# Performance work log

Hardware: AMD Instinct MI355X
Metric: run time of the kernel (lower is better)

The kernel has to match this reference:

```python
import jax, jax.numpy as jnp
import numpy as np

DIM = 1024
INNER = int(DIM * 1.5)
EPS = 1e-6


def setup_inputs() -> dict:
    key = jax.random.key(0)
    ks = jax.random.split(key, 8)
    B, L, D = 4, 2048, DIM
    s1 = 1.0 / np.sqrt(D)
    s2 = 1.0 / np.sqrt(INNER)
    return {
        "x": jax.random.normal(ks[0], (B, L, D), jnp.float32),
        "W1": jax.random.normal(ks[1], (D, INNER), jnp.float32) * s1,
        "b1": jnp.zeros((INNER,), jnp.float32),
        "W2": jax.random.normal(ks[2], (INNER, 3 * D), jnp.float32) * s2,
        "b2": jnp.zeros((3 * D,), jnp.float32),
        "Wv": jax.random.normal(ks[3], (D, D), jnp.float32) * (0.5 * s1),
        "bv": jnp.zeros((D,), jnp.float32),
        "mix_weight": jnp.full((D,), 0.5, jnp.float32),
        "norm_weight": jnp.ones((D,), jnp.float32),
    }


def rmsnorm(x, w):
    norm = jnp.sqrt(jnp.mean(x * x, axis=-1, keepdims=True) + EPS)
    return x / norm * w


def reference(x, W1, b1, W2, b2, Wv, bv, mix_weight, norm_weight):
    B, L, D = x.shape
    h = jax.nn.silu(x @ W1 + b1)              # [B,L,inner]
    qkg = h @ W2 + b2                          # [B,L,3D]
    q, k, g = jnp.split(qkg, 3, axis=-1)
    scores = jnp.einsum('bld,bmd->blm', q, k) / jnp.sqrt(jnp.float32(D))
    attn = jax.nn.softmax(scores, axis=-1)
    v = (x @ Wv + bv) * jax.nn.sigmoid(g)      # gated values [B,L,D]
    global_info = jnp.einsum('blm,bmd->bld', attn, v)
    output = mix_weight * global_info + (1.0 - mix_weight) * x
    return rmsnorm(output, norm_weight)
```

## Files before the change

### kernel.cpp

```cpp
#include <hip/hip_runtime.h>
#include <hip/hip_bf16.h>
#include <stdint.h>


typedef __bf16 bf16x8 __attribute__((ext_vector_type(8)));
typedef float f32x4 __attribute__((ext_vector_type(4)));

#define VM4 asm volatile("s_waitcnt vmcnt(4)" ::: "memory")
#define VM2 asm volatile("s_waitcnt vmcnt(2)" ::: "memory")
#define VM0 asm volatile("s_waitcnt vmcnt(0)" ::: "memory")
#define LGKM0 asm volatile("s_waitcnt lgkmcnt(0)" ::: "memory")
#define BAR __builtin_amdgcn_s_barrier()
#define SCB __builtin_amdgcn_sched_barrier(0)

__device__ __forceinline__ unsigned short f2bf(float f) {
    unsigned int u = __float_as_uint(f);
    u += 0x7fffu + ((u >> 16) & 1u);
    return (unsigned short)(u >> 16);
}
__device__ __forceinline__ float bf2f(unsigned short s) {
    return __uint_as_float(((unsigned int)s) << 16);
}
__device__ __forceinline__ void llds16(const void* g, void* l) {
    __builtin_amdgcn_global_load_lds(
        (const __attribute__((address_space(1))) void*)g,
        (__attribute__((address_space(3))) void*)l, 16, 0, 0);
}
__device__ __forceinline__ f32x4 MF(bf16x8 a, bf16x8 b, f32x4 c) {
    return __builtin_amdgcn_mfma_f32_16x16x32_bf16(a, b, c, 0, 0, 0);
}

__global__ __launch_bounds__(256) void cvt_f32_bf16(
    const float* __restrict__ in, unsigned short* __restrict__ out, long long n8) {
    long long i = (long long)blockIdx.x * 256 + threadIdx.x;
    if (i >= n8) return;
    float4 a = ((const float4*)in)[2 * i];
    float4 b = ((const float4*)in)[2 * i + 1];
    ushort4 p0, p1;
    p0.x = f2bf(a.x); p0.y = f2bf(a.y); p0.z = f2bf(a.z); p0.w = f2bf(a.w);
    p1.x = f2bf(b.x); p1.y = f2bf(b.y); p1.z = f2bf(b.z); p1.w = f2bf(b.w);
    ((ushort4*)out)[2 * i] = p0;
    ((ushort4*)out)[2 * i + 1] = p1;
}

__global__ __launch_bounds__(256) void transpose_cvt(
    const float* __restrict__ in, unsigned short* __restrict__ out, int R, int C) {
    __shared__ unsigned short tile[32][33];
    int c0 = blockIdx.x * 32, r0 = blockIdx.y * 32;
    int cc = threadIdx.x & 31, rr = threadIdx.x >> 5;
#pragma unroll
    for (int p = 0; p < 4; ++p) {
        int r = rr + p * 8;
        tile[r][cc] = f2bf(in[(size_t)(r0 + r) * C + c0 + cc]);
    }
    __syncthreads();
#pragma unroll
    for (int p = 0; p < 4; ++p) {
        int c = rr + p * 8;
        out[(size_t)(c0 + c) * R + r0 + cc] = tile[cc][c];
    }
}

template <int EPI>
__global__ __launch_bounds__(512, 1) void gemm5(
    const unsigned short* __restrict__ A, int lda, long long Abs,
    const unsigned short* __restrict__ B, int ldb, long long Bbs,
    int K,
    void* __restrict__ out, int ldo, long long Obs,
    const float* __restrict__ bias,
    const unsigned short* __restrict__ gate, int ldg,
    const float* __restrict__ xres, const float* __restrict__ mix,
    float scale, int gx) {
    __shared__ unsigned short lds[49152];
    const int tid = threadIdx.x, lane = tid & 63, wid = tid >> 6;
    const int wr = wid >> 1, wc = wid & 1;
    const int nwg = gridDim.x;
    const int bswz = ((int)blockIdx.x & 7) * (nwg >> 3) + ((int)blockIdx.x >> 3);
    const int bx = bswz % gx, by = bswz / gx;
    const int bm = by * 256, bn = bx * 128;
    const int z = blockIdx.z;
    A += (long long)z * Abs;
    B += (long long)z * Bbs;
    const int NT = K >> 6;

    const int sswz = ((tid & 7) ^ ((tid >> 3) & 7)) * 8;
    size_t agc[4], bgc[2];
#pragma unroll
    for (int c = 0; c < 4; ++c)
        agc[c] = (size_t)(bm + c * 64 + (tid >> 3)) * lda + sswz;
#pragma unroll
    for (int c = 0; c < 2; ++c)
        bgc[c] = (size_t)(bn + c * 64 + (tid >> 3)) * ldb + sswz;
    const int wl = wid * 512;

    auto stA01 = [&](int t, int buf) {
        const size_t k0 = (size_t)t << 6;
        llds16(A + agc[0] + k0, &lds[buf + wl]);
        llds16(A + agc[1] + k0, &lds[buf + 4096 + wl]);
    };
    auto stA23 = [&](int t, int buf) {
        const size_t k0 = (size_t)t << 6;
        llds16(A + agc[2] + k0, &lds[buf + 8192 + wl]);
        llds16(A + agc[3] + k0, &lds[buf + 12288 + wl]);
    };
    auto stB = [&](int t, int buf) {
        const size_t k0 = (size_t)t << 6;
        llds16(B + bgc[0] + k0, &lds[buf + 16384 + wl]);
        llds16(B + bgc[1] + k0, &lds[buf + 20480 + wl]);
    };

    const int l15 = lane & 15, g4 = lane >> 4, l7 = lane & 7;
    const int x0 = (g4 ^ l7) * 8, x1 = ((4 + g4) ^ l7) * 8;
    const int ab = (wr * 64 + l15) * 64;
    const int bbv = 16384 + (wc * 64 + l15) * 64;
    constexpr int X = 0, Y = 24576;

    f32x4 acc[4][4] = {};

    stB(0, X); stA01(0, X); stA23(0, X); stB(1, Y);
    VM4;
    BAR; SCB;

    int t = 0;
    while (true) {
        const bool last = (t + 2) >= NT;
        bf16x8 bf[4][2], af[2][2];
#pragma unroll
        for (int j = 0; j < 4; ++j) {
            bf[j][0] = *(const bf16x8*)&lds[X + bbv + j * 1024 + x0];
            bf[j][1] = *(const bf16x8*)&lds[X + bbv + j * 1024 + x1];
        }
#pragma unroll
        for (int i = 0; i < 2; ++i) {
            af[i][0] = *(const bf16x8*)&lds[X + ab + i * 1024 + x0];
            af[i][1] = *(const bf16x8*)&lds[X + ab + i * 1024 + x1];
        }
        stA01(t + 1, Y);
        LGKM0; SCB;
        __builtin_amdgcn_s_setprio(1);
#pragma unroll
        for (int s = 0; s < 2; ++s)
#pragma unroll
            for (int i = 0; i < 2; ++i)
#pragma unroll
                for (int j = 0; j < 4; ++j)
                    acc[i][j] = MF(af[i][s], bf[j][s], acc[i][j]);
        __builtin_amdgcn_s_setprio(0);
        VM4;
        BAR; SCB;
#pragma unroll
        for (int i = 0; i < 2; ++i) {
            af[i][0] = *(const bf16x8*)&lds[X + ab + (2 + i) * 1024 + x0];
            af[i][1] = *(const bf16x8*)&lds[X + ab + (2 + i) * 1024 + x1];
        }
        stA23(t + 1, Y);
        if (!last) stB(t + 2, X);
        LGKM0; SCB;
        __builtin_amdgcn_s_setprio(1);
#pragma unroll
        for (int s = 0; s < 2; ++s)
#pragma unroll
            for (int i = 0; i < 2; ++i)
#pragma unroll
                for (int j = 0; j < 4; ++j)
                    acc[2 + i][j] = MF(af[i][s], bf[j][s], acc[2 + i][j]);
        __builtin_amdgcn_s_setprio(0);
        if (last) { VM2; } else { VM4; }
        BAR; SCB;
#pragma unroll
        for (int j = 0; j < 4; ++j) {
            bf[j][0] = *(const bf16x8*)&lds[Y + bbv + j * 1024 + x0];
            bf[j][1] = *(const bf16x8*)&lds[Y + bbv + j * 1024 + x1];
        }
#pragma unroll
        for (int i = 0; i < 2; ++i) {
            af[i][0] = *(const bf16x8*)&lds[Y + ab + i * 1024 + x0];
            af[i][1] = *(const bf16x8*)&lds[Y + ab + i * 1024 + x1];
        }
        if (!last) stA01(t + 2, X);
        LGKM0; SCB;
        __builtin_amdgcn_s_setprio(1);
#pragma unroll
        for (int s = 0; s < 2; ++s)
#pragma unroll
            for (int i = 0; i < 2; ++i)
#pragma unroll
                for (int j = 0; j < 4; ++j)
                    acc[i][j] = MF(af[i][s], bf[j][s], acc[i][j]);
        __builtin_amdgcn_s_setprio(0);
        if (last) { VM0; } else { VM4; }
        BAR; SCB;
#pragma unroll
        for (int i = 0; i < 2; ++i) {
            af[i][0] = *(const bf16x8*)&lds[Y + ab + (2 + i) * 1024 + x0];
            af[i][1] = *(const bf16x8*)&lds[Y + ab + (2 + i) * 1024 + x1];
        }
        if (!last) { stA23(t + 2, X); stB(t + 3, Y); }
        LGKM0; SCB;
        __builtin_amdgcn_s_setprio(1);
#pragma unroll
        for (int s = 0; s < 2; ++s)
#pragma unroll
            for (int i = 0; i < 2; ++i)
#pragma unroll
                for (int j = 0; j < 4; ++j)
                    acc[2 + i][j] = MF(af[i][s], bf[j][s], acc[2 + i][j]);
        __builtin_amdgcn_s_setprio(0);
        if (last) break;
        VM4;
        BAR; SCB;
        t += 2;
    }

    const int row0 = bm + wr * 64, col0 = bn + wc * 64;
#pragma unroll
    for (int i = 0; i < 4; ++i) {
#pragma unroll
        for (int j = 0; j < 4; ++j) {
            const int n = col0 + j * 16 + l15;
            const int mb = row0 + i * 16 + g4 * 4;
            f32x4 v = acc[i][j];
            if constexpr (EPI == 1) {
                float bs = bias[n];
                unsigned short* o = (unsigned short*)out;
#pragma unroll
                for (int q = 0; q < 4; ++q)
                    o[(size_t)(mb + q) * ldo + n] = f2bf(v[q] + bs);
            } else if constexpr (EPI == 2) {
                float bs = bias[n];
                ushort4 pk;
                unsigned short* pku = (unsigned short*)&pk;
#pragma unroll
                for (int q = 0; q < 4; ++q) {
                    int m = mb + q;
                    float g = bf2f(gate[(size_t)m * ldg + n]);
                    pku[q] = f2bf((v[q] + bs) / (1.f + __expf(-g)));
                }
                unsigned short* o = (unsigned short*)out;
                size_t oi = ((size_t)(mb >> 11) * 1024 + n) * 2048 + (mb & 2047);
                *(ushort4*)(o + oi) = pk;
            } else if constexpr (EPI == 3) {
                float* o = (float*)out + (size_t)z * Obs;
#pragma unroll
                for (int q = 0; q < 4; ++q)
                    o[(size_t)(mb + q) * ldo + n] = v[q] * scale;
            } else {
                float* o = (float*)out + (size_t)z * Obs;
                const float* xr = xres + (size_t)z * Obs;
                float mw = mix[n];
#pragma unroll
                for (int q = 0; q < 4; ++q)
                    o[(size_t)(mb + q) * ldo + n] =
                        mw * v[q] + (1.f - mw) * xr[(size_t)(mb + q) * ldo + n];
            }
        }
    }
}

template <int EPI>
__global__ __launch_bounds__(256, 3) void gemmk(
    const unsigned short* __restrict__ A, int lda,
    const unsigned short* __restrict__ B, int ldb,
    int K, void* __restrict__ out, int ldo,
    const float* __restrict__ bias, int gx) {
    __shared__ unsigned short lds[24576];
    const int tid = threadIdx.x, lane = tid & 63, wid = tid >> 6;
    const int nwg = gridDim.x;
    const int bswz = ((int)blockIdx.x & 7) * (nwg >> 3) + ((int)blockIdx.x >> 3);
    const int bx = bswz % gx, by = bswz / gx;
    const int bm = by * 128, bn = bx * 128;
    const int NT = K >> 5;

    const int srow = tid >> 2;
    const int sswz = ((tid & 3) ^ ((tid >> 3) & 3)) * 8;
    size_t ag[2], bg[2];
    ag[0] = (size_t)(bm + srow) * lda + sswz;
    ag[1] = (size_t)(bm + 64 + srow) * lda + sswz;
    bg[0] = (size_t)(bn + srow) * ldb + sswz;
    bg[1] = (size_t)(bn + 64 + srow) * ldb + sswz;
    const int wl = wid * 512;

    auto stage = [&](int t, int bb) {
        const size_t k0 = (size_t)t << 5;
        llds16(A + ag[0] + k0, &lds[bb + wl]);
        llds16(A + ag[1] + k0, &lds[bb + 2048 + wl]);
        llds16(B + bg[0] + k0, &lds[bb + 4096 + wl]);
        llds16(B + bg[1] + k0, &lds[bb + 6144 + wl]);
    };

    const int wr = wid >> 1, wc = wid & 1;
    const int l15 = lane & 15, g4 = lane >> 4;
    const int fswz = (g4 ^ ((l15 >> 1) & 3)) * 8;
    const int aoff = (wr * 64 + l15) * 32 + fswz;
    const int boff = 4096 + (wc * 64 + l15) * 32 + fswz;

    f32x4 acc[4][4] = {};
    stage(0, 0);
    stage(1, 8192);
    VM4; BAR;

    int bb = 0;
    for (int t = 0; t < NT; ++t) {
        const bool st = (t + 2) < NT;
        if (st) {
            const int tgt = (bb >= 8192) ? bb - 8192 : bb + 16384;
            stage(t + 2, tgt);
        }
        SCB;
        bf16x8 af[4], bf[4];
#pragma unroll
        for (int i = 0; i < 4; ++i) {
            af[i] = *(const bf16x8*)&lds[bb + aoff + i * 512];
            bf[i] = *(const bf16x8*)&lds[bb + boff + i * 512];
        }
#pragma unroll
        for (int i = 0; i < 4; ++i)
#pragma unroll
            for (int j = 0; j < 4; ++j)
                acc[i][j] = MF(af[i], bf[j], acc[i][j]);
        LGKM0;
        if (st) { VM4; } else { VM0; }
        BAR;
        bb = (bb == 16384) ? 0 : bb + 8192;
    }

    const int row0 = bm + wr * 64, col0 = bn + wc * 64;
#pragma unroll
    for (int i = 0; i < 4; ++i) {
#pragma unroll
        for (int j = 0; j < 4; ++j) {
            const int n = col0 + j * 16 + l15;
            const int mb = row0 + i * 16 + g4 * 4;
            f32x4 v = acc[i][j];
            float bs = bias[n];
            unsigned short* o = (unsigned short*)out;
#pragma unroll
            for (int q = 0; q < 4; ++q) {
                float val = v[q] + bs;
                if constexpr (EPI == 0) val = val / (1.f + __expf(-val));
                o[(size_t)(mb + q) * ldo + n] = f2bf(val);
            }
        }
    }
}

__global__ __launch_bounds__(256) void softmax_inplace(float* __restrict__ scores) {
    const int L = 2048;
    float* sr = scores + (size_t)blockIdx.x * L;
    const int t = threadIdx.x, lane = t & 63, wid = t >> 6;
    float4 a = ((const float4*)sr)[2 * t];
    float4 b = ((const float4*)sr)[2 * t + 1];
    float vv[8] = {a.x, a.y, a.z, a.w, b.x, b.y, b.z, b.w};
    float mx = vv[0];
#pragma unroll
    for (int i = 1; i < 8; ++i) mx = fmaxf(mx, vv[i]);
#pragma unroll
    for (int off = 32; off; off >>= 1) mx = fmaxf(mx, __shfl_xor(mx, off));
    __shared__ float redm[4], reds[4];
    if (lane == 0) redm[wid] = mx;
    __syncthreads();
    mx = fmaxf(fmaxf(redm[0], redm[1]), fmaxf(redm[2], redm[3]));
    float s = 0.f;
#pragma unroll
    for (int i = 0; i < 8; ++i) {
        vv[i] = __expf(vv[i] - mx);
        s += vv[i];
    }
#pragma unroll
    for (int off = 32; off; off >>= 1) s += __shfl_xor(s, off);
    if (lane == 0) reds[wid] = s;
    __syncthreads();
    s = reds[0] + reds[1] + reds[2] + reds[3];
    float inv = 1.f / s;
    ushort4 p0, p1;
    unsigned short* pp0 = (unsigned short*)&p0;
    unsigned short* pp1 = (unsigned short*)&p1;
#pragma unroll
    for (int i = 0; i < 4; ++i) pp0[i] = f2bf(vv[i] * inv);
#pragma unroll
    for (int i = 0; i < 4; ++i) pp1[i] = f2bf(vv[4 + i] * inv);
    unsigned short* pr = (unsigned short*)sr;
    ((ushort4*)pr)[2 * t] = p0;
    ((ushort4*)pr)[2 * t + 1] = p1;
}

__global__ __launch_bounds__(256) void rmsnorm_inplace(
    float* __restrict__ io, const float* __restrict__ w) {
    const int D = 1024;
    float* r = io + (size_t)blockIdx.x * D;
    const int t = threadIdx.x, lane = t & 63, wid = t >> 6;
    float4 v = ((const float4*)r)[t];
    float ss = v.x * v.x + v.y * v.y + v.z * v.z + v.w * v.w;
#pragma unroll
    for (int off = 32; off; off >>= 1) ss += __shfl_xor(ss, off);
    __shared__ float red[4];
    if (lane == 0) red[wid] = ss;
    __syncthreads();
    ss = red[0] + red[1] + red[2] + red[3];
    float sc = rsqrtf(ss / (float)D + 1e-6f);
    float4 wv = ((const float4*)w)[t];
    v.x *= sc * wv.x; v.y *= sc * wv.y; v.z *= sc * wv.z; v.w *= sc * wv.w;
    ((float4*)r)[t] = v;
}

extern "C" void kernel_launch(void* const* d_in, const int* in_sizes, int n_in,
                              void* d_out, int out_size, void* d_ws, size_t ws_size,
                              hipStream_t stream) {
    const float* x = (const float*)d_in[0];
    const float* W1 = (const float*)d_in[1];
    const float* b1 = (const float*)d_in[2];
    const float* W2 = (const float*)d_in[3];
    const float* b2 = (const float*)d_in[4];
    const float* Wv = (const float*)d_in[5];
    const float* bv = (const float*)d_in[6];
    const float* mixw = (const float*)d_in[7];
    const float* normw = (const float*)d_in[8];
    float* out = (float*)d_out;

    const int L = 2048, D = 1024, INNER = 1536, BN4 = 4;
    const int M = BN4 * L;

    char* w = (char*)d_ws;
    auto carve = [&](size_t bytes) {
        void* p = (void*)w;
        w += (bytes + 255) & ~(size_t)255;
        return p;
    };
    unsigned short* xbf = (unsigned short*)carve((size_t)M * D * 2);
    unsigned short* w1t = (unsigned short*)carve((size_t)INNER * D * 2);
    unsigned short* w2t = (unsigned short*)carve((size_t)3 * D * INNER * 2);
    unsigned short* wvt = (unsigned short*)carve((size_t)D * D * 2);
    unsigned short* h = (unsigned short*)carve((size_t)M * INNER * 2);
    unsigned short* qkg = (unsigned short*)carve((size_t)M * 3 * D * 2);
    unsigned short* vt = (unsigned short*)carve((size_t)BN4 * D * L * 2);
    float* scores = (float*)carve((size_t)BN4 * L * L * 4);

    cvt_f32_bf16<<<(M * D) / 2048, 256, 0, stream>>>(x, xbf, (long long)M * D / 8);
    transpose_cvt<<<dim3(INNER / 32, D / 32), 256, 0, stream>>>(W1, w1t, D, INNER);
    transpose_cvt<<<dim3(3 * D / 32, INNER / 32), 256, 0, stream>>>(W2, w2t, INNER, 3 * D);
    transpose_cvt<<<dim3(D / 32, D / 32), 256, 0, stream>>>(Wv, wvt, D, D);
    gemmk<0><<<dim3(768, 1, 1), 256, 0, stream>>>(xbf, D, w1t, D, D, h, INNER,
                                                  b1, 12);
    gemm5<1><<<dim3(768, 1, 1), 512, 0, stream>>>(
        h, INNER, 0, w2t, INNER, 0, INNER, qkg, 3 * D, 0, b2, nullptr, 0,
        nullptr, nullptr, 1.f, 24);
    gemm5<2><<<dim3(256, 1, 1), 512, 0, stream>>>(
        xbf, D, 0, wvt, D, 0, D, vt, L, 0, bv, qkg + 2 * D, 3 * D, nullptr,
        nullptr, 1.f, 8);
    gemm5<3><<<dim3(128, 1, BN4), 512, 0, stream>>>(
        qkg, 3 * D, (long long)L * 3 * D, qkg + D, 3 * D, (long long)L * 3 * D,
        D, scores, L, (long long)L * L, nullptr, nullptr, 0, nullptr, nullptr,
        0.03125f, 16);
    softmax_inplace<<<BN4 * L, 256, 0, stream>>>(scores);
    gemm5<4><<<dim3(64, 1, BN4), 512, 0, stream>>>(
        (const unsigned short*)scores, 2 * L, (long long)L * 2 * L, vt, L,
        (long long)D * L, L, out, D, (long long)L * D, nullptr, nullptr, 0, x,
        mixw, 1.f, 8);
    rmsnorm_inplace<<<M, 256, 0, stream>>>(out, normw);
}
```

Measured before the change: 291.1 us.

## Fuse softmax into QK and PV GEMM epilogues using Cauchy-Schwarz max bound

Removes the separate softmax kernel and the fp32 score matrix. The QKG GEMM epilogue now accumulates per-row squared norms of q and k with atomics. A small kernel turns these into a per-batch upper bound on the scores (max|q|·max|k|/sqrt(D)). The QK GEMM then writes exp(score - bound) directly as bf16 and atomically accumulates row sums, and the PV GEMM divides by the row sum in its epilogue. This saves a full fp32 write, read and rewrite of the 4x2048x2048 score matrix. The risk is exp underflow when the bound is loose compared with the actual row max, plus atomic contention and the extra zeroing and bounds launches.

```diff
diff --git a/kernel.cpp b/kernel.cpp
--- a/kernel.cpp
+++ b/kernel.cpp
@@ -28,6 +28,11 @@
 }
 __device__ __forceinline__ f32x4 MF(bf16x8 a, bf16x8 b, f32x4 c) {
     return __builtin_amdgcn_mfma_f32_16x16x32_bf16(a, b, c, 0, 0, 0);
+}
+
+__global__ __launch_bounds__(256) void zero_f32(float* __restrict__ p, int n) {
+    int i = blockIdx.x * 256 + threadIdx.x;
+    if (i < n) p[i] = 0.f;
 }
 
 __global__ __launch_bounds__(256) void cvt_f32_bf16(
@@ -61,6 +66,30 @@
     }
 }
 
+__global__ __launch_bounds__(256) void bounds_kernel(
+    const float* __restrict__ nrm, float* __restrict__ bounds) {
+    const int z = blockIdx.x, t = threadIdx.x;
+    float qm = 0.f, km = 0.f;
+    for (int i = t; i < 2048; i += 256) {
+        qm = fmaxf(qm, nrm[z * 2048 + i]);
+        km = fmaxf(km, nrm[8192 + z * 2048 + i]);
+    }
+#pragma unroll
+    for (int off = 32; off; off >>= 1) {
+        qm = fmaxf(qm, __shfl_xor(qm, off));
+        km = fmaxf(km, __shfl_xor(km, off));
+    }
+    __shared__ float rq[4], rk[4];
+    const int lane = t & 63, wid = t >> 6;
+    if (lane == 0) { rq[wid] = qm; rk[wid] = km; }
+    __syncthreads();
+    if (t == 0) {
+        qm = fmaxf(fmaxf(rq[0], rq[1]), fmaxf(rq[2], rq[3]));
+        km = fmaxf(fmaxf(rk[0], rk[1]), fmaxf(rk[2], rk[3]));
+        bounds[z] = sqrtf(qm) * sqrtf(km) * 0.03125f;
+    }
+}
+
 template <int EPI>
 __global__ __launch_bounds__(512, 1) void gemm5(
     const unsigned short* __restrict__ A, int lda, long long Abs,
@@ -70,7 +99,8 @@
     const float* __restrict__ bias,
     const unsigned short* __restrict__ gate, int ldg,
     const float* __restrict__ xres, const float* __restrict__ mix,
-    float scale, int gx) {
+    float scale, int gx,
+    const float* __restrict__ bnd, float* __restrict__ stat) {
     __shared__ unsigned short lds[49152];
     const int tid = threadIdx.x, lane = tid & 63, wid = tid >> 6;
     const int wr = wid >> 1, wc = wid & 1;
@@ -213,45 +243,99 @@
     }
 
     const int row0 = bm + wr * 64, col0 = bn + wc * 64;
-#pragma unroll
-    for (int i = 0; i < 4; ++i) {
-#pragma unroll
-        for (int j = 0; j < 4; ++j) {
-            const int n = col0 + j * 16 + l15;
+    if constexpr (EPI == 1) {
+        unsigned short* o = (unsigned short*)out;
+        const int seg = col0 >> 10;
+#pragma unroll
+        for (int i = 0; i < 4; ++i) {
             const int mb = row0 + i * 16 + g4 * 4;
-            f32x4 v = acc[i][j];
-            if constexpr (EPI == 1) {
-                float bs = bias[n];
-                unsigned short* o = (unsigned short*)out;
-#pragma unroll
-                for (int q = 0; q < 4; ++q)
-                    o[(size_t)(mb + q) * ldo + n] = f2bf(v[q] + bs);
-            } else if constexpr (EPI == 2) {
-                float bs = bias[n];
+            float ssq[4] = {0.f, 0.f, 0.f, 0.f};
+#pragma unroll
+            for (int j = 0; j < 4; ++j) {
+                const int n = col0 + j * 16 + l15;
+                const float bs = bias[n];
+#pragma unroll
+                for (int q = 0; q < 4; ++q) {
+                    float val = acc[i][j][q] + bs;
+                    o[(size_t)(mb + q) * ldo + n] = f2bf(val);
+                    ssq[q] += val * val;
+                }
+            }
+            if (seg < 2) {
+#pragma unroll
+                for (int q = 0; q < 4; ++q) {
+                    float s = ssq[q];
+                    s += __shfl_xor(s, 1); s += __shfl_xor(s, 2);
+                    s += __shfl_xor(s, 4); s += __shfl_xor(s, 8);
+                    if (l15 == 0) atomicAdd(&stat[seg * 8192 + mb + q], s);
+                }
+            }
+        }
+    } else if constexpr (EPI == 2) {
+        unsigned short* o = (unsigned short*)out;
+#pragma unroll
+        for (int i = 0; i < 4; ++i) {
+            const int mb = row0 + i * 16 + g4 * 4;
+#pragma unroll
+            for (int j = 0; j < 4; ++j) {
+                const int n = col0 + j * 16 + l15;
+                const float bs = bias[n];
                 ushort4 pk;
                 unsigned short* pku = (unsigned short*)&pk;
 #pragma unroll
                 for (int q = 0; q < 4; ++q) {
                     int m = mb + q;
                     float g = bf2f(gate[(size_t)m * ldg + n]);
-                    pku[q] = f2bf((v[q] + bs) / (1.f + __expf(-g)));
+                    pku[q] = f2bf((acc[i][j][q] + bs) / (1.f + __expf(-g)));
                 }
-                unsigned short* o = (unsigned short*)out;
                 size_t oi = ((size_t)(mb >> 11) * 1024 + n) * 2048 + (mb & 2047);
                 *(ushort4*)(o + oi) = pk;
-            } else if constexpr (EPI == 3) {
-                float* o = (float*)out + (size_t)z * Obs;
-#pragma unroll
-                for (int q = 0; q < 4; ++q)
-                    o[(size_t)(mb + q) * ldo + n] = v[q] * scale;
-            } else {
-                float* o = (float*)out + (size_t)z * Obs;
-                const float* xr = xres + (size_t)z * Obs;
-                float mw = mix[n];
+            }
+        }
+    } else if constexpr (EPI == 5) {
+        unsigned short* o = (unsigned short*)out + (size_t)z * Obs;
+        const float Bz = bnd[z];
+#pragma unroll
+        for (int i = 0; i < 4; ++i) {
+            const int mb = row0 + i * 16 + g4 * 4;
+            float rs[4] = {0.f, 0.f, 0.f, 0.f};
+#pragma unroll
+            for (int j = 0; j < 4; ++j) {
+                const int n = col0 + j * 16 + l15;
+#pragma unroll
+                for (int q = 0; q < 4; ++q) {
+                    float p = __expf(acc[i][j][q] * scale - Bz);
+                    o[(size_t)(mb + q) * ldo + n] = f2bf(p);
+                    rs[q] += p;
+                }
+            }
+#pragma unroll
+            for (int q = 0; q < 4; ++q) {
+                float s = rs[q];
+                s += __shfl_xor(s, 1); s += __shfl_xor(s, 2);
+                s += __shfl_xor(s, 4); s += __shfl_xor(s, 8);
+                if (l15 == 0) atomicAdd(&stat[(size_t)z * 2048 + mb + q], s);
+            }
+        }
+    } else {
+        float* o = (float*)out + (size_t)z * Obs;
+        const float* xr = xres + (size_t)z * Obs;
+        const float* ls = bnd + (size_t)z * 2048;
+#pragma unroll
+        for (int i = 0; i < 4; ++i) {
+            const int mb = row0 + i * 16 + g4 * 4;
+            float invl[4];
+#pragma unroll
+            for (int q = 0; q < 4; ++q) invl[q] = 1.f / ls[mb + q];
+#pragma unroll
+            for (int j = 0; j < 4; ++j) {
+                const int n = col0 + j * 16 + l15;
+                const float mw = mix[n];
 #pragma unroll
                 for (int q = 0; q < 4; ++q)
                     o[(size_t)(mb + q) * ldo + n] =
-                        mw * v[q] + (1.f - mw) * xr[(size_t)(mb + q) * ldo + n];
+                        mw * (acc[i][j][q] * invl[q]) +
+                        (1.f - mw) * xr[(size_t)(mb + q) * ldo + n];
             }
         }
     }
@@ -344,46 +428,6 @@
     }
 }
 
-__global__ __launch_bounds__(256) void softmax_inplace(float* __restrict__ scores) {
-    const int L = 2048;
-    float* sr = scores + (size_t)blockIdx.x * L;
-    const int t = threadIdx.x, lane = t & 63, wid = t >> 6;
-    float4 a = ((const float4*)sr)[2 * t];
-    float4 b = ((const float4*)sr)[2 * t + 1];
-    float vv[8] = {a.x, a.y, a.z, a.w, b.x, b.y, b.z, b.w};
-    float mx = vv[0];
-#pragma unroll
-    for (int i = 1; i < 8; ++i) mx = fmaxf(mx, vv[i]);
-#pragma unroll
-    for (int off = 32; off; off >>= 1) mx = fmaxf(mx, __shfl_xor(mx, off));
-    __shared__ float redm[4], reds[4];
-    if (lane == 0) redm[wid] = mx;
-    __syncthreads();
-    mx = fmaxf(fmaxf(redm[0], redm[1]), fmaxf(redm[2], redm[3]));
-    float s = 0.f;
-#pragma unroll
-    for (int i = 0; i < 8; ++i) {
-        vv[i] = __expf(vv[i] - mx);
-        s += vv[i];
-    }
-#pragma unroll
-    for (int off = 32; off; off >>= 1) s += __shfl_xor(s, off);
-    if (lane == 0) reds[wid] = s;
-    __syncthreads();
-    s = reds[0] + reds[1] + reds[2] + reds[3];
-    float inv = 1.f / s;
-    ushort4 p0, p1;
-    unsigned short* pp0 = (unsigned short*)&p0;
-    unsigned short* pp1 = (unsigned short*)&p1;
-#pragma unroll
-    for (int i = 0; i < 4; ++i) pp0[i] = f2bf(vv[i] * inv);
-#pragma unroll
-    for (int i = 0; i < 4; ++i) pp1[i] = f2bf(vv[4 + i] * inv);
-    unsigned short* pr = (unsigned short*)sr;
-    ((ushort4*)pr)[2 * t] = p0;
-    ((ushort4*)pr)[2 * t + 1] = p1;
-}
-
 __global__ __launch_bounds__(256) void rmsnorm_inplace(
     float* __restrict__ io, const float* __restrict__ w) {
     const int D = 1024;
@@ -433,8 +477,12 @@
     unsigned short* h = (unsigned short*)carve((size_t)M * INNER * 2);
     unsigned short* qkg = (unsigned short*)carve((size_t)M * 3 * D * 2);
     unsigned short* vt = (unsigned short*)carve((size_t)BN4 * D * L * 2);
-    float* scores = (float*)carve((size_t)BN4 * L * L * 4);
-
+    unsigned short* pbuf = (unsigned short*)carve((size_t)BN4 * L * L * 2);
+    float* norm2 = (float*)carve((size_t)2 * M * 4);
+    float* lsum = (float*)carve((size_t)M * 4);
+    float* bounds = (float*)carve((size_t)BN4 * 4);
+
+    zero_f32<<<(3 * M) / 256, 256, 0, stream>>>(norm2, 3 * M);
     cvt_f32_bf16<<<(M * D) / 2048, 256, 0, stream>>>(x, xbf, (long long)M * D / 8);
     transpose_cvt<<<dim3(INNER / 32, D / 32), 256, 0, stream>>>(W1, w1t, D, INNER);
     transpose_cvt<<<dim3(3 * D / 32, INNER / 32), 256, 0, stream>>>(W2, w2t, INNER, 3 * D);
@@ -443,18 +491,17 @@
                                                   b1, 12);
     gemm5<1><<<dim3(768, 1, 1), 512, 0, stream>>>(
         h, INNER, 0, w2t, INNER, 0, INNER, qkg, 3 * D, 0, b2, nullptr, 0,
-        nullptr, nullptr, 1.f, 24);
+        nullptr, nullptr, 1.f, 24, nullptr, norm2);
+    bounds_kernel<<<BN4, 256, 0, stream>>>(norm2, bounds);
     gemm5<2><<<dim3(256, 1, 1), 512, 0, stream>>>(
         xbf, D, 0, wvt, D, 0, D, vt, L, 0, bv, qkg + 2 * D, 3 * D, nullptr,
-        nullptr, 1.f, 8);
-    gemm5<3><<<dim3(128, 1, BN4), 512, 0, stream>>>(
+        nullptr, 1.f, 8, nullptr, nullptr);
+    gemm5<5><<<dim3(128, 1, BN4), 512, 0, stream>>>(
         qkg, 3 * D, (long long)L * 3 * D, qkg + D, 3 * D, (long long)L * 3 * D,
-        D, scores, L, (long long)L * L, nullptr, nullptr, 0, nullptr, nullptr,
-        0.03125f, 16);
-    softmax_inplace<<<BN4 * L, 256, 0, stream>>>(scores);
-    gemm5<4><<<dim3(64, 1, BN4), 512, 0, stream>>>(
-        (const unsigned short*)scores, 2 * L, (long long)L * 2 * L, vt, L,
-        (long long)D * L, L, out, D, (long long)L * D, nullptr, nullptr, 0, x,
-        mixw, 1.f, 8);
+        D, pbuf, L, (long long)L * L, nullptr, nullptr, 0, nullptr, nullptr,
+        0.03125f, 16, bounds, lsum);
+    gemm5<6><<<dim3(64, 1, BN4), 512, 0, stream>>>(
+        pbuf, L, (long long)L * L, vt, L, (long long)D * L, L, out, D,
+        (long long)L * D, nullptr, nullptr, 0, x, mixw, 1.f, 8, lsum, nullptr);
     rmsnorm_inplace<<<M, 256, 0, stream>>>(out, normw);
 }
```

After: 282.3 us. -3.0%, faster.
